# Kernel tuning notes

Hardware: AMD Instinct MI355X
Metric: run time of the kernel (lower is better)

Reference implementation:

```python
import jax, jax.numpy as jnp
import numpy as np

G, C_PER, C_IN, J, B, H, W, K = 8, 32, 256, 64, 16, 56, 56, 3


def setup_inputs() -> dict:
    key = jax.random.key(0)
    kx, kw, kb = jax.random.split(key, 3)
    x = jax.random.normal(kx, (B, C_IN, H, W), dtype=jnp.float32)
    # Per-cluster conv weights [G, j_rank, c, K, K] and biases [G, j_rank]
    weight = jax.random.normal(kw, (G, J, C_PER, K, K), dtype=jnp.float32) * 0.05
    bias = jax.random.normal(kb, (G, J), dtype=jnp.float32) * 0.01
    # Arrangements: 8 clusters of 32 non-contiguous channel indices (fixed permutation)
    arrangements = jnp.asarray(
        np.random.RandomState(0).permutation(C_IN).reshape(G, C_PER), dtype=jnp.int32
    )
    return {"x": x, "weight": weight, "bias": bias, "arrangements": arrangements}


def reference(x, weight, bias, arrangements):
    # Gather channel subsets: x[:, arr] -> [B, G, c, H, W] -> [G, B, c, H, W]
    xg = jnp.transpose(x[:, arrangements], (1, 0, 2, 3, 4))

    def conv1(xi, wi):
        # xi: [B, c, H, W], wi: [J, c, K, K]; stride 1, pad 1, dilation 1 (torch default cross-correlation)
        return jax.lax.conv_general_dilated(
            xi, wi,
            window_strides=(1, 1),
            padding=((1, 1), (1, 1)),
            dimension_numbers=("NCHW", "OIHW", "NCHW"),
        )

    out = jax.vmap(conv1)(xg, weight)              # [G, B, J, H, W]
    out = out + bias[:, None, :, None, None]
    g, b, j, h, w = out.shape
    # torch.cat(dim=1) over clusters -> [B, G*J, H, W]
    return jnp.transpose(out, (1, 0, 2, 3, 4)).reshape(b, g * j, h, w)
```

## Files before the change

### kernel.cpp

```cpp
#include <hip/hip_runtime.h>


#define NG 8
#define CPER 32
#define CIN 256
#define NJ 64
#define NB 16
#define NH 56
#define NW 56
#define PXST 40
#define BUFSH (4 * 58 * PXST)
#define NPACK (16 * 4 * 58)
#define NITER 15
#define WEI_SH (9 * 2048)

typedef __attribute__((ext_vector_type(8))) short short8v;
typedef __attribute__((ext_vector_type(4))) float float4v;

__device__ __forceinline__ unsigned bf16rne(float f) {
    unsigned u = __float_as_uint(f);
    return (u + 0x7FFFu + ((u >> 16) & 1u)) >> 16;
}

__global__ __launch_bounds__(256, 2)
void gconv_mfma(const float* __restrict__ x,
                const float* __restrict__ w,
                const float* __restrict__ bias,
                const int* __restrict__ arr,
                float* __restrict__ out) {
    __shared__ __align__(16) unsigned short smem[2 * BUFSH];

    const int tid   = threadIdx.x;
    const int chunk = blockIdx.x;
    const int b     = blockIdx.y;
    const int g     = blockIdx.z;
    const int lane  = tid & 63;
    const int jt    = tid >> 6;
    const int n     = lane & 15;
    const int kq    = lane >> 4;

    {
        const float* wg = w + (size_t)g * (NJ * CPER * 9);
        for (int e = tid; e < WEI_SH; e += 256) {
            int jc = e / 9, tap = e - jc * 9;
            smem[tap * 2048 + jc] = (unsigned short)bf16rne(wg[e]);
        }
    }
    __syncthreads();
    short8v A[9];
    {
        const unsigned short* wl = smem + (jt * 16 + n) * CPER + kq * 8;
        #pragma unroll
        for (int t = 0; t < 9; ++t) A[t] = *(const short8v*)(wl + t * 2048);
    }
    float4v binit;
    #pragma unroll
    for (int i = 0; i < 4; ++i) binit[i] = bias[g * NJ + jt * 16 + kq * 4 + i];
    __syncthreads();

    int pre0[NITER], pre1[NITER], meta[NITER];
    #pragma unroll
    for (int k = 0; k < NITER; ++k) {
        int e = tid + 256 * k;
        int act = e < NPACK;
        int c2 = e / 232;
        int rem = e - c2 * 232;
        int row = rem / 58;
        int colp = rem - row * 58;
        int ch0 = 0, ch1 = 0;
        if (act) { ch0 = arr[g * CPER + c2 * 2]; ch1 = arr[g * CPER + c2 * 2 + 1]; }
        pre0[k] = ch0 * (NH * NW) + (row - 1) * NW + (colp - 1);
        pre1[k] = ch1 * (NH * NW) + (row - 1) * NW + (colp - 1);
        int cv = act && ((unsigned)(colp - 1) < NW);
        meta[k] = ((row * 58 + colp) * PXST + c2 * 2) | (row << 14) | (cv << 16) | (act << 17);
    }
    const float* xb = x + (size_t)b * (CIN * NH * NW);

    float f0[NITER], f1[NITER];
    int r0 = chunk * 14;

    {
        int roff = r0 * NW;
        #pragma unroll
        for (int k = 0; k < NITER; ++k) {
            int row = (meta[k] >> 14) & 3;
            int v = ((meta[k] >> 16) & 1) && ((unsigned)(r0 + row - 1) < NH);
            f0[k] = v ? xb[pre0[k] + roff] : 0.0f;
            f1[k] = v ? xb[pre1[k] + roff] : 0.0f;
        }
        #pragma unroll
        for (int k = 0; k < NITER; ++k) {
            if ((meta[k] >> 17) & 1)
                *(unsigned*)(&smem[meta[k] & 0x3FFF]) =
                    bf16rne(f0[k]) | (bf16rne(f1[k]) << 16);
        }
    }
    __syncthreads();

    for (int bd = 0; bd < 7; ++bd) {
        if (bd < 6) {
            int r1 = r0 + 2, roff = r1 * NW;
            #pragma unroll
            for (int k = 0; k < NITER; ++k) {
                int row = (meta[k] >> 14) & 3;
                int v = ((meta[k] >> 16) & 1) && ((unsigned)(r1 + row - 1) < NH);
                f0[k] = v ? xb[pre0[k] + roff] : 0.0f;
                f1[k] = v ? xb[pre1[k] + roff] : 0.0f;
            }
        }
        {
            const unsigned short* buf = smem + (bd & 1) * BUFSH;
            const int obase = ((b * (NG * NJ) + g * NJ + jt * 16 + kq * 4) * NH + r0) * NW;
            int rl = 0, col = n;
            #pragma unroll
            for (int tp = 0; tp < 3; ++tp) {
                int rlA = rl, colA = col; col += 16; if (col >= NW) { col -= NW; ++rl; }
                int rlB = rl, colB = col; col += 16; if (col >= NW) { col -= NW; ++rl; }
                const unsigned short* pA = buf + (rlA * 58 + colA) * PXST + kq * 8;
                const unsigned short* pB = buf + (rlB * 58 + colB) * PXST + kq * 8;
                float4v a0 = binit, a1 = binit;
                #pragma unroll
                for (int kh = 0; kh < 3; ++kh)
                    #pragma unroll
                    for (int kw = 0; kw < 3; ++kw) {
                        short8v b0 = *(const short8v*)(pA + (kh * 58 + kw) * PXST);
                        short8v b1 = *(const short8v*)(pB + (kh * 58 + kw) * PXST);
                        a0 = __builtin_amdgcn_mfma_f32_16x16x32_bf16(A[kh * 3 + kw], b0, a0, 0, 0, 0);
                        a1 = __builtin_amdgcn_mfma_f32_16x16x32_bf16(A[kh * 3 + kw], b1, a1, 0, 0, 0);
                    }
                int obA = obase + rlA * NW + colA;
                int obB = obase + rlB * NW + colB;
                #pragma unroll
                for (int i = 0; i < 4; ++i) {
                    out[obA + i * (NH * NW)] = a0[i];
                    out[obB + i * (NH * NW)] = a1[i];
                }
            }
            const unsigned short* pA = buf + (rl * 58 + col) * PXST + kq * 8;
            float4v a0 = binit;
            #pragma unroll
            for (int kh = 0; kh < 3; ++kh)
                #pragma unroll
                for (int kw = 0; kw < 3; ++kw) {
                    short8v b0 = *(const short8v*)(pA + (kh * 58 + kw) * PXST);
                    a0 = __builtin_amdgcn_mfma_f32_16x16x32_bf16(A[kh * 3 + kw], b0, a0, 0, 0, 0);
                }
            int obA = obase + rl * NW + col;
            #pragma unroll
            for (int i = 0; i < 4; ++i) out[obA + i * (NH * NW)] = a0[i];
        }
        if (bd < 6) {
            unsigned short* dst = smem + ((bd + 1) & 1) * BUFSH;
            #pragma unroll
            for (int k = 0; k < NITER; ++k) {
                if ((meta[k] >> 17) & 1)
                    *(unsigned*)(&dst[meta[k] & 0x3FFF]) =
                        bf16rne(f0[k]) | (bf16rne(f1[k]) << 16);
            }
            r0 += 2;
            __syncthreads();
        }
    }
}

extern "C" void kernel_launch(void* const* d_in, const int* in_sizes, int n_in,
                              void* d_out, int out_size, void* d_ws, size_t ws_size,
                              hipStream_t stream) {
    const float* x    = (const float*)d_in[0];
    const float* wght = (const float*)d_in[1];
    const float* bias = (const float*)d_in[2];
    const int*   arr  = (const int*)d_in[3];
    float* out = (float*)d_out;

    dim3 grid(4, NB, NG);
    gconv_mfma<<<grid, 256, 0, stream>>>(x, wght, bias, arr, out);
}
```

Before: 184.5 us.

## Retile grouped conv: 2x2 MFMA register blocking per wave, more row chunks

```diff
diff --git a/kernel.cpp b/kernel.cpp
--- a/kernel.cpp
+++ b/kernel.cpp
@@ -8,6 +8,7 @@
 #define NB 16
 #define NH 56
 #define NW 56
+#define HW (NH * NW)
 #define PXST 40
 #define BUFSH (4 * 58 * PXST)
 #define NPACK (16 * 4 * 58)
@@ -22,7 +23,7 @@
     return (u + 0x7FFFu + ((u >> 16) & 1u)) >> 16;
 }
 
-__global__ __launch_bounds__(256, 2)
+__global__ __launch_bounds__(256, 3)
 void gconv_mfma(const float* __restrict__ x,
                 const float* __restrict__ w,
                 const float* __restrict__ bias,
@@ -35,129 +36,199 @@
     const int b     = blockIdx.y;
     const int g     = blockIdx.z;
     const int lane  = tid & 63;
-    const int jt    = tid >> 6;
+    const int wid   = tid >> 6;
+    const int jp    = wid & 1;
+    const int th    = wid >> 1;
     const int n     = lane & 15;
     const int kq    = lane >> 4;
-
-    {
-        const float* wg = w + (size_t)g * (NJ * CPER * 9);
-        for (int e = tid; e < WEI_SH; e += 256) {
-            int jc = e / 9, tap = e - jc * 9;
-            smem[tap * 2048 + jc] = (unsigned short)bf16rne(wg[e]);
-        }
-    }
-    __syncthreads();
-    short8v A[9];
-    {
-        const unsigned short* wl = smem + (jt * 16 + n) * CPER + kq * 8;
-        #pragma unroll
-        for (int t = 0; t < 9; ++t) A[t] = *(const short8v*)(wl + t * 2048);
-    }
-    float4v binit;
-    #pragma unroll
-    for (int i = 0; i < 4; ++i) binit[i] = bias[g * NJ + jt * 16 + kq * 4 + i];
-    __syncthreads();
-
-    int pre0[NITER], pre1[NITER], meta[NITER];
+    const int r0c   = chunk * 8;
+
+    const float* xb = x + (size_t)b * (CIN * HW);
+
+    int pre0[NITER], meta[NITER];
     #pragma unroll
     for (int k = 0; k < NITER; ++k) {
         int e = tid + 256 * k;
-        int act = e < NPACK;
-        int c2 = e / 232;
-        int rem = e - c2 * 232;
-        int row = rem / 58;
+        bool act = (k < 14) || (tid < NPACK - 3584);
+        int c2   = e / 232;
+        int rem  = e - c2 * 232;
+        int row  = rem / 58;
         int colp = rem - row * 58;
-        int ch0 = 0, ch1 = 0;
-        if (act) { ch0 = arr[g * CPER + c2 * 2]; ch1 = arr[g * CPER + c2 * 2 + 1]; }
-        pre0[k] = ch0 * (NH * NW) + (row - 1) * NW + (colp - 1);
-        pre1[k] = ch1 * (NH * NW) + (row - 1) * NW + (colp - 1);
-        int cv = act && ((unsigned)(colp - 1) < NW);
-        meta[k] = ((row * 58 + colp) * PXST + c2 * 2) | (row << 14) | (cv << 16) | (act << 17);
-    }
-    const float* xb = x + (size_t)b * (CIN * NH * NW);
+        int ch0 = 0, dch = 0;
+        if (act) {
+            int i0 = arr[g * CPER + 2 * c2];
+            int i1 = arr[g * CPER + 2 * c2 + 1];
+            ch0 = i0; dch = i1 - i0;
+        }
+        pre0[k] = ch0 * HW + (row - 1) * NW + (colp - 1);
+        int cv = ((unsigned)(colp - 1) < (unsigned)NW) ? 1 : 0;
+        meta[k] = ((row * 58 + colp) * PXST + c2 * 2) | (row << 14)
+                | (cv << 16) | ((dch & 0x3FF) << 18);
+    }
 
     float f0[NITER], f1[NITER];
-    int r0 = chunk * 14;
-
     {
-        int roff = r0 * NW;
+        int roff = r0c * NW;
         #pragma unroll
         for (int k = 0; k < NITER; ++k) {
-            int row = (meta[k] >> 14) & 3;
-            int v = ((meta[k] >> 16) & 1) && ((unsigned)(r0 + row - 1) < NH);
-            f0[k] = v ? xb[pre0[k] + roff] : 0.0f;
-            f1[k] = v ? xb[pre1[k] + roff] : 0.0f;
-        }
+            int m = meta[k];
+            int row = (m >> 14) & 3;
+            bool v = (m & (1 << 16)) && ((unsigned)(r0c - 1 + row) < (unsigned)NH);
+            if (k == 14 && tid >= NPACK - 3584) v = false;
+            int off = pre0[k] + roff;
+            int dch = (m << 4) >> 22;
+            f0[k] = v ? xb[off] : 0.0f;
+            f1[k] = v ? xb[off + dch * HW] : 0.0f;
+        }
+    }
+
+    {
+        const float* wg = w + (size_t)g * (NJ * CPER * 9);
         #pragma unroll
-        for (int k = 0; k < NITER; ++k) {
-            if ((meta[k] >> 17) & 1)
-                *(unsigned*)(&smem[meta[k] & 0x3FFF]) =
-                    bf16rne(f0[k]) | (bf16rne(f1[k]) << 16);
+        for (int it = 0; it < WEI_SH / 256; ++it) {
+            int e   = tid + it * 256;
+            int tap = e >> 11;
+            int jc  = e & 2047;
+            smem[tap * 2048 + jc] = (unsigned short)bf16rne(wg[jc * 9 + tap]);
         }
     }
     __syncthreads();
 
-    for (int bd = 0; bd < 7; ++bd) {
-        if (bd < 6) {
-            int r1 = r0 + 2, roff = r1 * NW;
+    short8v A0[9], A1[9];
+    {
+        const unsigned short* wl = smem + (jp * 32 + n) * CPER + kq * 8;
+        #pragma unroll
+        for (int t = 0; t < 9; ++t) {
+            A0[t] = *(const short8v*)(wl + t * 2048);
+            A1[t] = *(const short8v*)(wl + t * 2048 + 16 * CPER);
+        }
+    }
+    float4v binit0, binit1;
+    #pragma unroll
+    for (int i = 0; i < 4; ++i) {
+        binit0[i] = bias[g * NJ + jp * 32 + kq * 4 + i];
+        binit1[i] = bias[g * NJ + jp * 32 + 16 + kq * 4 + i];
+    }
+    __syncthreads();
+
+    #pragma unroll
+    for (int k = 0; k < NITER; ++k) {
+        if (k < 14 || tid < NPACK - 3584)
+            *(unsigned*)(&smem[meta[k] & 0x3FFF]) =
+                bf16rne(f0[k]) | (bf16rne(f1[k]) << 16);
+    }
+    __syncthreads();
+
+    const int obase = ((b * (NG * NJ) + g * NJ + jp * 32 + kq * 4) * NH + r0c) * NW;
+
+    for (int bd = 0; bd < 4; ++bd) {
+        if (bd < 3) {
+            int rb = r0c + (bd + 1) * 2;
+            int roff = rb * NW;
             #pragma unroll
             for (int k = 0; k < NITER; ++k) {
-                int row = (meta[k] >> 14) & 3;
-                int v = ((meta[k] >> 16) & 1) && ((unsigned)(r1 + row - 1) < NH);
-                f0[k] = v ? xb[pre0[k] + roff] : 0.0f;
-                f1[k] = v ? xb[pre1[k] + roff] : 0.0f;
+                int m = meta[k];
+                int row = (m >> 14) & 3;
+                bool v = (m & (1 << 16)) && ((unsigned)(rb - 1 + row) < (unsigned)NH);
+                if (k == 14 && tid >= NPACK - 3584) v = false;
+                int off = pre0[k] + roff;
+                int dch = (m << 4) >> 22;
+                f0[k] = v ? xb[off] : 0.0f;
+                f1[k] = v ? xb[off + dch * HW] : 0.0f;
             }
         }
         {
             const unsigned short* buf = smem + (bd & 1) * BUFSH;
-            const int obase = ((b * (NG * NJ) + g * NJ + jt * 16 + kq * 4) * NH + r0) * NW;
-            int rl = 0, col = n;
-            #pragma unroll
-            for (int tp = 0; tp < 3; ++tp) {
-                int rlA = rl, colA = col; col += 16; if (col >= NW) { col -= NW; ++rl; }
-                int rlB = rl, colB = col; col += 16; if (col >= NW) { col -= NW; ++rl; }
-                const unsigned short* pA = buf + (rlA * 58 + colA) * PXST + kq * 8;
-                const unsigned short* pB = buf + (rlB * 58 + colB) * PXST + kq * 8;
-                float4v a0 = binit, a1 = binit;
+            const int ob = obase + bd * 2 * NW;
+            if (th == 0) {
                 #pragma unroll
-                for (int kh = 0; kh < 3; ++kh)
-                    #pragma unroll
-                    for (int kw = 0; kw < 3; ++kw) {
-                        short8v b0 = *(const short8v*)(pA + (kh * 58 + kw) * PXST);
-                        short8v b1 = *(const short8v*)(pB + (kh * 58 + kw) * PXST);
-                        a0 = __builtin_amdgcn_mfma_f32_16x16x32_bf16(A[kh * 3 + kw], b0, a0, 0, 0, 0);
-                        a1 = __builtin_amdgcn_mfma_f32_16x16x32_bf16(A[kh * 3 + kw], b1, a1, 0, 0, 0);
+                for (int t0 = 0; t0 < 4; t0 += 2) {
+                    int pA = t0 * 16 + n;  int rlA = pA >= NW; int colA = pA - rlA * NW;
+                    int pB = pA + 16;      int rlB = pB >= NW; int colB = pB - rlB * NW;
+                    const unsigned short* bpA = buf + (rlA * 58 + colA) * PXST + kq * 8;
+                    const unsigned short* bpB = buf + (rlB * 58 + colB) * PXST + kq * 8;
+                    float4v a00 = binit0, a01 = binit1, a10 = binit0, a11 = binit1;
+                    #pragma unroll
+                    for (int kh = 0; kh < 3; ++kh)
+                        #pragma unroll
+                        for (int kw = 0; kw < 3; ++kw) {
+                            const int tap = kh * 3 + kw;
+                            short8v vA = *(const short8v*)(bpA + (kh * 58 + kw) * PXST);
+                            short8v vB = *(const short8v*)(bpB + (kh * 58 + kw) * PXST);
+                            a00 = __builtin_amdgcn_mfma_f32_16x16x32_bf16(A0[tap], vA, a00, 0, 0, 0);
+                            a01 = __builtin_amdgcn_mfma_f32_16x16x32_bf16(A1[tap], vA, a01, 0, 0, 0);
+                            a10 = __builtin_amdgcn_mfma_f32_16x16x32_bf16(A0[tap], vB, a10, 0, 0, 0);
+                            a11 = __builtin_amdgcn_mfma_f32_16x16x32_bf16(A1[tap], vB, a11, 0, 0, 0);
+                        }
+                    int oA = ob + rlA * NW + colA;
+                    int oB = ob + rlB * NW + colB;
+                    #pragma unroll
+                    for (int i = 0; i < 4; ++i) {
+                        out[oA + i * HW]        = a00[i];
+                        out[oA + (16 + i) * HW] = a01[i];
+                        out[oB + i * HW]        = a10[i];
+                        out[oB + (16 + i) * HW] = a11[i];
                     }
-                int obA = obase + rlA * NW + colA;
-                int obB = obase + rlB * NW + colB;
-                #pragma unroll
-                for (int i = 0; i < 4; ++i) {
-                    out[obA + i * (NH * NW)] = a0[i];
-                    out[obB + i * (NH * NW)] = a1[i];
+                }
+            } else {
+                {
+                    int pA = 4 * 16 + n;   int rlA = pA >= NW; int colA = pA - rlA * NW;
+                    int pB = pA + 16;      int rlB = pB >= NW; int colB = pB - rlB * NW;
+                    const unsigned short* bpA = buf + (rlA * 58 + colA) * PXST + kq * 8;
+                    const unsigned short* bpB = buf + (rlB * 58 + colB) * PXST + kq * 8;
+                    float4v a00 = binit0, a01 = binit1, a10 = binit0, a11 = binit1;
+                    #pragma unroll
+                    for (int kh = 0; kh < 3; ++kh)
+                        #pragma unroll
+                        for (int kw = 0; kw < 3; ++kw) {
+                            const int tap = kh * 3 + kw;
+                            short8v vA = *(const short8v*)(bpA + (kh * 58 + kw) * PXST);
+                            short8v vB = *(const short8v*)(bpB + (kh * 58 + kw) * PXST);
+                            a00 = __builtin_amdgcn_mfma_f32_16x16x32_bf16(A0[tap], vA, a00, 0, 0, 0);
+                            a01 = __builtin_amdgcn_mfma_f32_16x16x32_bf16(A1[tap], vA, a01, 0, 0, 0);
+                            a10 = __builtin_amdgcn_mfma_f32_16x16x32_bf16(A0[tap], vB, a10, 0, 0, 0);
+                            a11 = __builtin_amdgcn_mfma_f32_16x16x32_bf16(A1[tap], vB, a11, 0, 0, 0);
+                        }
+                    int oA = ob + rlA * NW + colA;
+                    int oB = ob + rlB * NW + colB;
+                    #pragma unroll
+                    for (int i = 0; i < 4; ++i) {
+                        out[oA + i * HW]        = a00[i];
+                        out[oA + (16 + i) * HW] = a01[i];
+                        out[oB + i * HW]        = a10[i];
+                        out[oB + (16 + i) * HW] = a11[i];
+                    }
+                }
+                {
+                    int pA = 6 * 16 + n;   int rlA = pA >= NW; int colA = pA - rlA * NW;
+                    const unsigned short* bpA = buf + (rlA * 58 + colA) * PXST + kq * 8;
+                    float4v a00 = binit0, a01 = binit1;
+                    #pragma unroll
+                    for (int kh = 0; kh < 3; ++kh)
+                        #pragma unroll
+                        for (int kw = 0; kw < 3; ++kw) {
+                            const int tap = kh * 3 + kw;
+                            short8v vA = *(const short8v*)(bpA + (kh * 58 + kw) * PXST);
+                            a00 = __builtin_amdgcn_mfma_f32_16x16x32_bf16(A0[tap], vA, a00, 0, 0, 0);
+                            a01 = __builtin_amdgcn_mfma_f32_16x16x32_bf16(A1[tap], vA, a01, 0, 0, 0);
+                        }
+                    int oA = ob + rlA * NW + colA;
+                    #pragma unroll
+                    for (int i = 0; i < 4; ++i) {
+                        out[oA + i * HW]        = a00[i];
+                        out[oA + (16 + i) * HW] = a01[i];
+                    }
                 }
             }
-            const unsigned short* pA = buf + (rl * 58 + col) * PXST + kq * 8;
-            float4v a0 = binit;
-            #pragma unroll
-            for (int kh = 0; kh < 3; ++kh)
-                #pragma unroll
-                for (int kw = 0; kw < 3; ++kw) {
-                    short8v b0 = *(const short8v*)(pA + (kh * 58 + kw) * PXST);
-                    a0 = __builtin_amdgcn_mfma_f32_16x16x32_bf16(A[kh * 3 + kw], b0, a0, 0, 0, 0);
-                }
-            int obA = obase + rl * NW + col;
-            #pragma unroll
-            for (int i = 0; i < 4; ++i) out[obA + i * (NH * NW)] = a0[i];
-        }
-        if (bd < 6) {
+        }
+        if (bd < 3) {
             unsigned short* dst = smem + ((bd + 1) & 1) * BUFSH;
             #pragma unroll
             for (int k = 0; k < NITER; ++k) {
-                if ((meta[k] >> 17) & 1)
+                if (k < 14 || tid < NPACK - 3584)
                     *(unsigned*)(&dst[meta[k] & 0x3FFF]) =
                         bf16rne(f0[k]) | (bf16rne(f1[k]) << 16);
             }
-            r0 += 2;
             __syncthreads();
         }
     }
@@ -172,6 +243,6 @@
     const int*   arr  = (const int*)d_in[3];
     float* out = (float*)d_out;
 
-    dim3 grid(4, NB, NG);
+    dim3 grid(7, NB, NG);
     gconv_mfma<<<grid, 256, 0, stream>>>(x, wght, bias, arr, out);
 }
```

New measurement: 415.6 us. +125.3%, slower.
